# Kernel optimization log

Hardware: AMD Instinct MI355X
Metric: run time of the kernel (lower is better)

The kernel has to match this reference:

```python
import jax, jax.numpy as jnp
import numpy as np

NUM_CLASSES = 5  # original computes int(mask.max())+1 at runtime; labels are drawn in [0,5) so this is 5.
EPS = 1e-07


def setup_inputs() -> dict:
    key = jax.random.key(0)
    k1, k2 = jax.random.split(key)
    output = jax.random.randint(k1, (128, 1, 512, 512), 0, NUM_CLASSES).astype(jnp.float32)
    mask = jax.random.randint(k2, (1, 128, 512, 512), 0, NUM_CLASSES).astype(jnp.int32)
    return {"output": output, "mask": mask}


def reference(output, mask):
    # Squeeze to [D, H, W] volumes, as the torch module does.
    p = jnp.squeeze(output, 1)          # [D, H, W] float labels
    m = jnp.squeeze(mask, 0)            # [D, H, W] int labels

    pi = p.astype(jnp.int32).ravel()    # predicted class per voxel
    mi = m.ravel()                      # target class per voxel

    ones = jnp.ones(pi.shape, dtype=jnp.float32)
    # den1[i] = sum((p==i)^2) = count of voxels predicted i  (single pass histogram)
    den1 = jax.ops.segment_sum(ones, pi, num_segments=NUM_CLASSES)
    # den2[i] = count of voxels labeled i
    den2 = jax.ops.segment_sum(ones, mi, num_segments=NUM_CLASSES)
    # num[i]  = count of voxels where prediction == label == i
    agree = (pi == mi).astype(jnp.float32)
    num = jax.ops.segment_sum(agree, pi, num_segments=NUM_CLASSES)

    dice = 2.0 * ((num + EPS) / (den1 + den2 + EPS))   # [NUM_CLASSES]
    return jnp.sum(dice) / NUM_CLASSES
```

## Files before the change

### kernel.cpp

```cpp
#include <hip/hip_runtime.h>

#define NC 5
#define DICE_EPS 1e-7f

typedef unsigned long long u64;
typedef unsigned int u32;


#define BLOCKS 2048
#define CHUNK  4096

__device__ __forceinline__ void accum4(float4 pf, int4 mv,
                                       u64& A1, u64& A2, u64& AN)
{
    int p0 = (int)pf.x, p1 = (int)pf.y, p2 = (int)pf.z, p3 = (int)pf.w;
    int s0 = p0 << 3, s1 = p1 << 3, s2 = p2 << 3, s3 = p3 << 3;
    A1 += (1ull << s0) + (1ull << s1) + (1ull << s2) + (1ull << s3);
    A2 += (1ull << (mv.x << 3)) + (1ull << (mv.y << 3)) +
          (1ull << (mv.z << 3)) + (1ull << (mv.w << 3));
    AN += (1ull << (p0 == mv.x ? s0 : 40)) +
          (1ull << (p1 == mv.y ? s1 : 40)) +
          (1ull << (p2 == mv.z ? s2 : 40)) +
          (1ull << (p3 == mv.w ? s3 : 40));
}

#define FLUSH()                                                         \
    do {                                                                \
        _Pragma("unroll")                                               \
        for (int c = 0; c < NC; ++c) {                                  \
            den1[c] += (u32)(A1 >> (8 * c)) & 0xFF;                     \
            den2[c] += (u32)(A2 >> (8 * c)) & 0xFF;                     \
            num [c] += (u32)(AN >> (8 * c)) & 0xFF;                     \
        }                                                               \
        A1 = 0; A2 = 0; AN = 0;                                         \
    } while (0)

__global__ __launch_bounds__(256) void dice_hist_kernel(
    const float* __restrict__ pred_f, const int* __restrict__ mask,
    u32* __restrict__ cnt, int n)
{
    u32 den1[NC] = {0, 0, 0, 0, 0};
    u32 den2[NC] = {0, 0, 0, 0, 0};
    u32 num [NC] = {0, 0, 0, 0, 0};

    const int tid = threadIdx.x;
    const int n4  = n >> 2;

    const float4* __restrict__ p4 = (const float4*)pred_f;
    const int4*   __restrict__ m4 = (const int4*)mask;

    u64 A1 = 0, A2 = 0, AN = 0;

    if (n4 == (int)gridDim.x * CHUNK) {
        const int base = blockIdx.x * CHUNK + tid;
        #pragma unroll 4
        for (int k = 0; k < CHUNK / 256; ++k) {
            int i = base + k * 256;
            accum4(p4[i], m4[i], A1, A2, AN);
        }
        FLUSH();
    } else {
        const int nt = gridDim.x * blockDim.x;
        int i = blockIdx.x * blockDim.x + tid;
        int cin = 0;
        for (; i < n4; i += nt) {
            accum4(p4[i], m4[i], A1, A2, AN);
            cin += 4;
            if (cin >= 224) { FLUSH(); cin = 0; }
        }
        FLUSH();
        for (int j = (n4 << 2) + blockIdx.x * blockDim.x + tid; j < n; j += nt) {
            int p = (int)pred_f[j];
            int m = mask[j];
            #pragma unroll
            for (int c = 0; c < NC; ++c) {
                u32 a = (p == c), b = (m == c);
                den1[c] += a;
                den2[c] += b;
                num [c] += a & b;
            }
        }
    }

    #pragma unroll
    for (int c = 0; c < NC; ++c) {
        #pragma unroll
        for (int off = 32; off > 0; off >>= 1) {
            den1[c] += __shfl_xor(den1[c], off, 64);
            den2[c] += __shfl_xor(den2[c], off, 64);
            num [c] += __shfl_xor(num [c], off, 64);
        }
    }

    __shared__ u32 s_cnt[3 * NC];
    if (tid < 3 * NC) s_cnt[tid] = 0;
    __syncthreads();

    if ((tid & 63) == 0) {
        #pragma unroll
        for (int c = 0; c < NC; ++c) {
            atomicAdd(&s_cnt[c],          den1[c]);
            atomicAdd(&s_cnt[NC + c],     den2[c]);
            atomicAdd(&s_cnt[2 * NC + c], num [c]);
        }
    }
    __syncthreads();

    if (tid < 3 * NC) {
        atomicAdd(&cnt[tid * 16], s_cnt[tid]);
    }
}

__global__ void dice_final_kernel(const u32* __restrict__ cnt,
                                  float* __restrict__ out)
{
    if (blockIdx.x == 0 && threadIdx.x == 0) {
        float s = 0.0f;
        #pragma unroll
        for (int c = 0; c < NC; ++c) {
            float d1 = (float)cnt[c * 16];
            float d2 = (float)cnt[(NC + c) * 16];
            float nm = (float)cnt[(2 * NC + c) * 16];
            s += 2.0f * ((nm + DICE_EPS) / (d1 + d2 + DICE_EPS));
        }
        out[0] = s / (float)NC;
    }
}

extern "C" void kernel_launch(void* const* d_in, const int* in_sizes, int n_in,
                              void* d_out, int out_size, void* d_ws, size_t ws_size,
                              hipStream_t stream) {
    const float* pred = (const float*)d_in[0];
    const int*   mask = (const int*)d_in[1];
    const int n = in_sizes[0];

    u32* cnt = (u32*)d_ws;
    hipMemsetAsync(d_ws, 0, 256 * sizeof(u32), stream);

    dice_hist_kernel<<<BLOCKS, 256, 0, stream>>>(pred, mask, cnt, n);
    dice_final_kernel<<<1, 64, 0, stream>>>(cnt, (float*)d_out);
}
```

Baseline: 282.4 us.

## Use wave-strided grid with batched nontemporal loads and fewer blocks

Halves the grid to 1024 blocks and has each wave walk eight grid-strided groups, issuing eight 16-byte nontemporal loads up front per group before any arithmetic. A sched_barrier keeps the compiler from interleaving the loads with the histogram work, so more memory requests are in flight per wave. Nontemporal hints aim to avoid polluting caches with streaming data. Per-thread counts stay at 128 elements before flush, so the 8-bit packed counters do not overflow. Fewer blocks may reduce latency hiding if occupancy drops.

```diff
diff --git a/kernel.cpp b/kernel.cpp
--- a/kernel.cpp
+++ b/kernel.cpp
@@ -5,12 +5,14 @@
 
 typedef unsigned long long u64;
 typedef unsigned int u32;
+typedef float v4f __attribute__((ext_vector_type(4)));
+typedef int   v4i __attribute__((ext_vector_type(4)));
 
 
-#define BLOCKS 2048
-#define CHUNK  4096
+#define BLOCKS 1024
+#define GROUPS 8
 
-__device__ __forceinline__ void accum4(float4 pf, int4 mv,
+__device__ __forceinline__ void accum4(v4f pf, v4i mv,
                                        u64& A1, u64& A2, u64& AN)
 {
     int p0 = (int)pf.x, p1 = (int)pf.y, p2 = (int)pf.z, p3 = (int)pf.w;
@@ -46,17 +48,32 @@
     const int tid = threadIdx.x;
     const int n4  = n >> 2;
 
-    const float4* __restrict__ p4 = (const float4*)pred_f;
-    const int4*   __restrict__ m4 = (const int4*)mask;
+    const v4f* __restrict__ p4 = (const v4f*)pred_f;
+    const v4i* __restrict__ m4 = (const v4i*)mask;
 
     u64 A1 = 0, A2 = 0, AN = 0;
 
-    if (n4 == (int)gridDim.x * CHUNK) {
-        const int base = blockIdx.x * CHUNK + tid;
-        #pragma unroll 4
-        for (int k = 0; k < CHUNK / 256; ++k) {
-            int i = base + k * 256;
-            accum4(p4[i], m4[i], A1, A2, AN);
+    const int totalWaves = (int)(gridDim.x * blockDim.x) >> 6;
+    const int gstride    = totalWaves * 256;
+
+    if (n4 == gstride * GROUPS) {
+        const int W    = ((int)(blockIdx.x * blockDim.x) + tid) >> 6;
+        const int lane = tid & 63;
+        int base = W * 256 + lane;
+        for (int g = 0; g < GROUPS; ++g, base += gstride) {
+            v4f a0 = __builtin_nontemporal_load(p4 + base);
+            v4f a1 = __builtin_nontemporal_load(p4 + base + 64);
+            v4f a2 = __builtin_nontemporal_load(p4 + base + 128);
+            v4f a3 = __builtin_nontemporal_load(p4 + base + 192);
+            v4i b0 = __builtin_nontemporal_load(m4 + base);
+            v4i b1 = __builtin_nontemporal_load(m4 + base + 64);
+            v4i b2 = __builtin_nontemporal_load(m4 + base + 128);
+            v4i b3 = __builtin_nontemporal_load(m4 + base + 192);
+            __builtin_amdgcn_sched_barrier(0);
+            accum4(a0, b0, A1, A2, AN);
+            accum4(a1, b1, A1, A2, AN);
+            accum4(a2, b2, A1, A2, AN);
+            accum4(a3, b3, A1, A2, AN);
         }
         FLUSH();
     } else {
```

New measurement: 254.3 us. -10.0%, faster.
